# Kernel optimization log

Measured on AMD Instinct MI355X. Metric: run time of the kernel, lower is better.

## Reference

```python
import jax, jax.numpy as jnp
import numpy as np

N_NODES = 1_000_000
N_EDGES = 16_000_000
D = 2          # num_dimensions (hard-coded in source)
H = 64         # hidden_channnels
G = 1024       # number of graphs in the batch


def setup_inputs() -> dict:
    key = jax.random.key(0)
    ks = jax.random.split(key, 10)
    x = jax.random.normal(ks[0], (N_NODES, D), dtype=jnp.float32)
    edge_index = jax.random.randint(ks[1], (2, N_EDGES), 0, N_NODES, dtype=jnp.int64)
    batch = jnp.sort(jax.random.randint(ks[2], (N_NODES,), 0, G, dtype=jnp.int64))
    s = 0.5
    return {
        "x": x,
        "lin_w": jax.random.normal(ks[3], (D, D), dtype=jnp.float32) * s,
        "lin_b": jnp.zeros((D,), jnp.float32),
        "gn_weight": jnp.ones((D,), jnp.float32),
        "gn_bias": jnp.zeros((D,), jnp.float32),
        "gn_mean_scale": jnp.ones((D,), jnp.float32),
        "gcn_w": jax.random.normal(ks[4], (D, D), dtype=jnp.float32) * s,
        "gcn_b": jnp.zeros((D,), jnp.float32),
        "fc1_w": jax.random.normal(ks[5], (H, D), dtype=jnp.float32) * s,
        "fc1_b": jnp.zeros((H,), jnp.float32),
        "fc2_w": jax.random.normal(ks[6], (D, H), dtype=jnp.float32) * (1.0 / np.sqrt(H)),
        "fc2_b": jnp.zeros((D,), jnp.float32),
        "edge_index": edge_index,
        "batch": batch,
    }


def reference(x, lin_w, lin_b, gn_weight, gn_bias, gn_mean_scale,
              gcn_w, gcn_b, fc1_w, fc1_b, fc2_w, fc2_b, edge_index, batch):
    n = x.shape[0]
    # lin
    h = x @ lin_w.T + lin_b
    # GraphNorm called without batch -> single-graph stats; eps = num_dimensions = 2 (arg-order quirk)
    mean = h.mean(axis=0)
    out = h - mean * gn_mean_scale
    var = (out * out).mean(axis=0)
    h = gn_weight * out * jax.lax.rsqrt(var + jnp.float32(D)) + gn_bias
    h = jax.nn.relu(h)
    # GCNConv (add_self_loops=True, sym norm) + residual
    row, col = edge_index[0], edge_index[1]
    deg = jax.ops.segment_sum(jnp.ones_like(col, dtype=h.dtype), col, num_segments=n) + 1.0
    dis = jax.lax.rsqrt(deg)                       # deg^{-1/2}
    hw = h @ gcn_w.T                               # [N, D]
    msg = (dis[row] * dis[col])[:, None] * hw[row] # [E, D]
    agg = jax.ops.segment_sum(msg, col, num_segments=n)
    conv = agg + hw / deg[:, None] + gcn_b         # self-loop term = dis_i^2 * hw_i
    h = conv + h
    # fc1
    h = h @ fc1_w.T + fc1_b                        # [N, H]
    # InstanceNorm1d on 2D input -> unbatched (C=N, L=H): per-row norm over H; eps = H (arg-order quirk)
    m = h.mean(axis=1, keepdims=True)
    v = ((h - m) ** 2).mean(axis=1, keepdims=True)
    h = (h - m) * jax.lax.rsqrt(v + jnp.float32(H))
    # fc2
    h = h @ fc2_w.T + fc2_b                        # [N, D]
    # scatter_mean over batch
    ssum = jax.ops.segment_sum(h, batch, num_segments=G)
    cnt = jax.ops.segment_sum(jnp.ones((n,), h.dtype), batch, num_segments=G)
    return ssum / jnp.maximum(cnt, 1.0)[:, None]
```

## Files before the change

kernel.cpp:

```cpp
#include <hip/hip_runtime.h>

#define BLK 256
#define CH 8192
#define BSHIFT 12
#define BRANGE 4096
#define BMASK 4095
#define NSB 512


__global__ void k_stats_hist(const float* __restrict__ x, int n,
                             const int* __restrict__ col, int E, int NB,
                             double* __restrict__ partials, int* __restrict__ bhist) {
    __shared__ int h[256];
    for (int j = threadIdx.x; j < 256; j += blockDim.x) h[j] = 0;
    __syncthreads();
    int stride = gridDim.x * blockDim.x;
    int gtid = blockIdx.x * blockDim.x + threadIdx.x;

    int nqe = E >> 2;
    for (int q = gtid; q < nqe; q += stride) {
        int4 c = reinterpret_cast<const int4*>(col)[q];
        atomicAdd(&h[c.x >> BSHIFT], 1);
        atomicAdd(&h[c.y >> BSHIFT], 1);
        atomicAdd(&h[c.z >> BSHIFT], 1);
        atomicAdd(&h[c.w >> BSHIFT], 1);
    }
    if (blockIdx.x == 0) {
        for (int e = (nqe << 2) + threadIdx.x; e < E; e += blockDim.x)
            atomicAdd(&h[col[e] >> BSHIFT], 1);
    }

    float s0 = 0.f, s1 = 0.f, s2 = 0.f, s3 = 0.f, s4 = 0.f;
    int nv = n >> 1;
    for (int i = gtid; i < nv; i += stride) {
        float4 v = reinterpret_cast<const float4*>(x)[i];
        s0 += v.x + v.z; s1 += v.y + v.w;
        s2 += v.x * v.x + v.z * v.z;
        s3 += v.y * v.y + v.w * v.w;
        s4 += v.x * v.y + v.z * v.w;
    }
    if (blockIdx.x == 0 && threadIdx.x == 0 && (n & 1)) {
        float2 v = reinterpret_cast<const float2*>(x)[n - 1];
        s0 += v.x; s1 += v.y; s2 += v.x * v.x; s3 += v.y * v.y; s4 += v.x * v.y;
    }
    for (int off = 32; off; off >>= 1) {
        s0 += __shfl_down(s0, off);
        s1 += __shfl_down(s1, off);
        s2 += __shfl_down(s2, off);
        s3 += __shfl_down(s3, off);
        s4 += __shfl_down(s4, off);
    }
    __shared__ double lds[4][5];
    int wid = threadIdx.x >> 6;
    if ((threadIdx.x & 63) == 0) {
        lds[wid][0] = s0; lds[wid][1] = s1; lds[wid][2] = s2;
        lds[wid][3] = s3; lds[wid][4] = s4;
    }
    __syncthreads();
    if (threadIdx.x == 0) {
        double t0 = 0, t1 = 0, t2 = 0, t3 = 0, t4 = 0;
        for (int w = 0; w < 4; ++w) {
            t0 += lds[w][0]; t1 += lds[w][1]; t2 += lds[w][2];
            t3 += lds[w][3]; t4 += lds[w][4];
        }
        double* o = partials + (size_t)blockIdx.x * 5;
        o[0] = t0; o[1] = t1; o[2] = t2; o[3] = t3; o[4] = t4;
    }
    for (int j = threadIdx.x; j < NB; j += blockDim.x)
        if (h[j]) atomicAdd(&bhist[j], h[j]);
}


__global__ void k_params(const double* __restrict__ partials, int np,
                         const int* __restrict__ bhist, int NB,
                         int* __restrict__ gbase, int* __restrict__ cursor,
                         const float* lin_w, const float* lin_b,
                         const float* gn_w, const float* gn_b, const float* gn_ms,
                         const float* gcn_w, const float* gcn_b,
                         const float* fc1_w, const float* fc1_b,
                         const float* fc2_w, const float* fc2_b,
                         int n, float* __restrict__ P) {
    int tid = threadIdx.x;
    if (bhist) {
        __shared__ int si[256];
        int hv = (tid < NB) ? bhist[tid] : 0;
        si[tid] = hv; __syncthreads();
        for (int off = 1; off < 256; off <<= 1) {
            int t = (tid >= off) ? si[tid - off] : 0;
            __syncthreads();
            si[tid] += t;
            __syncthreads();
        }
        if (tid < NB) { gbase[tid] = si[tid] - hv; cursor[tid] = si[tid] - hv; }
        if (tid == 0) gbase[NB] = si[255];
        __syncthreads();
    }
    double a0 = 0, a1 = 0, a2 = 0, a3 = 0, a4 = 0;
    for (int i = tid; i < np; i += blockDim.x) {
        const double* q = partials + (size_t)i * 5;
        a0 += q[0]; a1 += q[1]; a2 += q[2]; a3 += q[3]; a4 += q[4];
    }
    for (int off = 32; off; off >>= 1) {
        a0 += __shfl_down(a0, off);
        a1 += __shfl_down(a1, off);
        a2 += __shfl_down(a2, off);
        a3 += __shfl_down(a3, off);
        a4 += __shfl_down(a4, off);
    }
    __shared__ double red[4][5];
    int wid = tid >> 6;
    if ((tid & 63) == 0) {
        red[wid][0] = a0; red[wid][1] = a1; red[wid][2] = a2;
        red[wid][3] = a3; red[wid][4] = a4;
    }
    __syncthreads();
    if (tid != 0) return;
    double Sx0 = 0, Sx1 = 0, Sxx = 0, Syy = 0, Sxy = 0;
    for (int w = 0; w < 4; ++w) {
        Sx0 += red[w][0]; Sx1 += red[w][1]; Sxx += red[w][2];
        Syy += red[w][3]; Sxy += red[w][4];
    }
    double N = (double)n;
    for (int c = 0; c < 2; ++c) {
        double L0 = lin_w[c * 2], L1 = lin_w[c * 2 + 1], lb = lin_b[c];
        double m   = (L0 * Sx0 + L1 * Sx1) / N + lb;
        double Eh2 = (L0 * L0 * Sxx + L1 * L1 * Syy + 2.0 * L0 * L1 * Sxy
                      + 2.0 * lb * (L0 * Sx0 + L1 * Sx1)) / N + lb * lb;
        double s   = gn_ms[c];
        double var = Eh2 - 2.0 * s * m * m + s * s * m * m;
        double inv = 1.0 / sqrt(var + 2.0);
        double gam = gn_w[c];
        P[c * 2 + 0] = (float)(gam * inv * L0);
        P[c * 2 + 1] = (float)(gam * inv * L1);
        P[4 + c]     = (float)(gam * inv * (lb - m * s) + gn_b[c]);
    }
    P[6] = gcn_w[0]; P[7] = gcn_w[1]; P[8] = gcn_w[2]; P[9] = gcn_w[3];
    P[10] = gcn_b[0]; P[11] = gcn_b[1];
    double b0 = 0, b1 = 0, bb = 0;
    for (int j = 0; j < 64; ++j) { b0 += fc1_w[2 * j]; b1 += fc1_w[2 * j + 1]; bb += fc1_b[j]; }
    b0 /= 64.0; b1 /= 64.0; bb /= 64.0;
    double S00 = 0, S01 = 0, S11 = 0, Sb0 = 0, Sb1 = 0, Sbb = 0;
    double M00 = 0, M01 = 0, M10 = 0, M11 = 0, t0 = 0, t1 = 0;
    for (int j = 0; j < 64; ++j) {
        double w0 = fc1_w[2 * j] - b0, w1 = fc1_w[2 * j + 1] - b1, b = fc1_b[j] - bb;
        S00 += w0 * w0; S01 += w0 * w1; S11 += w1 * w1;
        Sb0 += w0 * b;  Sb1 += w1 * b;  Sbb += b * b;
        double f0 = fc2_w[j], f1 = fc2_w[64 + j];
        M00 += f0 * w0; M01 += f0 * w1; t0 += f0 * b;
        M10 += f1 * w0; M11 += f1 * w1; t1 += f1 * b;
    }
    P[12] = (float)(S00 / 64.0); P[13] = (float)(S01 / 64.0); P[14] = (float)(S11 / 64.0);
    P[15] = (float)(Sb0 / 64.0); P[16] = (float)(Sb1 / 64.0); P[17] = (float)(Sbb / 64.0);
    P[18] = (float)M00; P[19] = (float)M01; P[20] = (float)M10; P[21] = (float)M11;
    P[22] = (float)t0;  P[23] = (float)t1;
    P[24] = fc2_b[0];   P[25] = fc2_b[1];
}


__global__ void k_hist(const int* __restrict__ col, int E, int NB, int* __restrict__ bhist) {
    __shared__ int h[256];
    for (int j = threadIdx.x; j < 256; j += blockDim.x) h[j] = 0;
    __syncthreads();
    int nq = E >> 2;
    int stride = gridDim.x * blockDim.x;
    for (int q = blockIdx.x * blockDim.x + threadIdx.x; q < nq; q += stride) {
        int4 c = reinterpret_cast<const int4*>(col)[q];
        atomicAdd(&h[c.x >> BSHIFT], 1);
        atomicAdd(&h[c.y >> BSHIFT], 1);
        atomicAdd(&h[c.z >> BSHIFT], 1);
        atomicAdd(&h[c.w >> BSHIFT], 1);
    }
    if (blockIdx.x == 0) {
        for (int e = (nq << 2) + threadIdx.x; e < E; e += blockDim.x)
            atomicAdd(&h[col[e] >> BSHIFT], 1);
    }
    __syncthreads();
    for (int j = threadIdx.x; j < NB; j += blockDim.x)
        if (h[j]) atomicAdd(&bhist[j], h[j]);
}

__global__ __launch_bounds__(256) void k_binA(const int* __restrict__ row,
                                              const int* __restrict__ col, int E,
                                              int NB, int* __restrict__ cursor,
                                              unsigned* __restrict__ staging) {
    __shared__ unsigned buf[CH];
    __shared__ int h[256], si[256], lpos[256], lcur[256];
    int tid = threadIdx.x;
    int start = blockIdx.x * CH;
    int end = start + CH; if (end > E) end = E;
    h[tid] = 0;
    __syncthreads();
    for (int e = start + tid; e < end; e += 256)
        atomicAdd(&h[col[e] >> BSHIFT], 1);
    __syncthreads();
    int hv = h[tid];
    si[tid] = hv; __syncthreads();
    for (int off = 1; off < 256; off <<= 1) {
        int t = (tid >= off) ? si[tid - off] : 0;
        __syncthreads();
        si[tid] += t;
        __syncthreads();
    }
    lpos[tid] = si[tid] - hv;
    lcur[tid] = (tid < NB && hv) ? atomicAdd(&cursor[tid], hv) : 0;
    __syncthreads();
    for (int e = start + tid; e < end; e += 256) {
        int c = col[e];
        unsigned w = ((unsigned)row[e] << BSHIFT) | (unsigned)(c & BMASK);
        int slot = atomicAdd(&lpos[c >> BSHIFT], 1);
        buf[slot] = w;
    }
    __syncthreads();
    int wid = tid >> 6, lane = tid & 63;
    for (int b = wid; b < NB; b += 4) {
        int m = h[b];
        if (!m) continue;
        int lb = si[b] - m;
        int g = lcur[b];
        for (int k = lane; k < m; k += 64)
            staging[g + k] = buf[lb + k];
    }
}

__global__ __launch_bounds__(1024) void k_degprep(const unsigned* __restrict__ staging,
                                                  const int* __restrict__ gbase,
                                                  const float* __restrict__ x,
                                                  const float* __restrict__ P,
                                                  int n, int* __restrict__ deg,
                                                  float2* __restrict__ p) {
    __shared__ int hist[BRANGE];
    int tid = threadIdx.x;
    for (int j = tid; j < BRANGE; j += 1024) hist[j] = 0;
    __syncthreads();
    int s = gbase[blockIdx.x], e = gbase[blockIdx.x + 1];
    int pre = (4 - (s & 3)) & 3; int cnt = e - s; if (pre > cnt) pre = cnt;
    for (int i = s + tid; i < s + pre; i += 1024)
        atomicAdd(&hist[staging[i] & BMASK], 1);
    int vs = s + pre;
    int nq = (e - vs) >> 2;
    const uint4* sv = reinterpret_cast<const uint4*>(staging + vs);
    for (int q = tid; q < nq; q += 1024) {
        uint4 w = sv[q];
        atomicAdd(&hist[w.x & BMASK], 1);
        atomicAdd(&hist[w.y & BMASK], 1);
        atomicAdd(&hist[w.z & BMASK], 1);
        atomicAdd(&hist[w.w & BMASK], 1);
    }
    for (int i = vs + (nq << 2) + tid; i < e; i += 1024)
        atomicAdd(&hist[staging[i] & BMASK], 1);
    __syncthreads();
    float A00 = P[0], A01 = P[1], A10 = P[2], A11 = P[3], q0 = P[4], q1 = P[5];
    float g00 = P[6], g01 = P[7], g10 = P[8], g11 = P[9];
    int nb = blockIdx.x << BSHIFT;
    int lim = n - nb; if (lim > BRANGE) lim = BRANGE;
    for (int j = tid; j < lim; j += 1024) {
        int d = hist[j];
        deg[nb + j] = d;
        float2 v = reinterpret_cast<const float2*>(x)[nb + j];
        float gg0 = fmaxf(fmaf(A00, v.x, fmaf(A01, v.y, q0)), 0.f);
        float gg1 = fmaxf(fmaf(A10, v.x, fmaf(A11, v.y, q1)), 0.f);
        float hw0 = g00 * gg0 + g01 * gg1;
        float hw1 = g10 * gg0 + g11 * gg1;
        float degf = (float)d + 1.0f;
        float dis = rsqrtf(degf);
        p[nb + j] = make_float2(dis * hw0, dis * hw1);
    }
}

#define AGG2(W, PV) \
    atomicAdd(&acc[2 * ((W) & BMASK)],     (PV).x); \
    atomicAdd(&acc[2 * ((W) & BMASK) + 1], (PV).y);

__global__ __launch_bounds__(1024) void k_agg(
        const unsigned* __restrict__ staging, const int* __restrict__ gbase,
        const float2* __restrict__ p, float* __restrict__ pacc) {
    __shared__ float acc[2 * BRANGE];
    int tid = threadIdx.x;
    for (int j = tid; j < 2 * BRANGE; j += 1024) acc[j] = 0.f;
    __syncthreads();
    int b = blockIdx.x >> 1, half = blockIdx.x & 1;
    int s0 = gbase[b], e0 = gbase[b + 1];
    int hc = (e0 - s0) >> 1;
    int s = s0 + half * hc;
    int e = half ? e0 : (s0 + hc);
    int cnt = e - s;
    int pre = (4 - (s & 3)) & 3; if (pre > cnt) pre = cnt;
    for (int i = s + tid; i < s + pre; i += 1024) {
        unsigned w = staging[i]; float2 pv = p[w >> BSHIFT];
        AGG2(w, pv)
    }
    int vs = s + pre;
    int nq = (e - vs) >> 2;
    const uint4* sv = reinterpret_cast<const uint4*>(staging + vs);
    int q = tid;
    for (; q + 3 * 1024 < nq; q += 4 * 1024) {
        uint4 wa = sv[q];
        uint4 wb = sv[q + 1024];
        uint4 wc = sv[q + 2048];
        uint4 wd = sv[q + 3072];
        float2 a0 = p[wa.x >> BSHIFT], a1 = p[wa.y >> BSHIFT];
        float2 a2 = p[wa.z >> BSHIFT], a3 = p[wa.w >> BSHIFT];
        float2 b0 = p[wb.x >> BSHIFT], b1 = p[wb.y >> BSHIFT];
        float2 b2 = p[wb.z >> BSHIFT], b3 = p[wb.w >> BSHIFT];
        float2 c0 = p[wc.x >> BSHIFT], c1 = p[wc.y >> BSHIFT];
        float2 c2 = p[wc.z >> BSHIFT], c3 = p[wc.w >> BSHIFT];
        float2 d0 = p[wd.x >> BSHIFT], d1 = p[wd.y >> BSHIFT];
        float2 d2 = p[wd.z >> BSHIFT], d3 = p[wd.w >> BSHIFT];
        AGG2(wa.x, a0) AGG2(wa.y, a1) AGG2(wa.z, a2) AGG2(wa.w, a3)
        AGG2(wb.x, b0) AGG2(wb.y, b1) AGG2(wb.z, b2) AGG2(wb.w, b3)
        AGG2(wc.x, c0) AGG2(wc.y, c1) AGG2(wc.z, c2) AGG2(wc.w, c3)
        AGG2(wd.x, d0) AGG2(wd.y, d1) AGG2(wd.z, d2) AGG2(wd.w, d3)
    }
    for (; q < nq; q += 1024) {
        uint4 w = sv[q];
        float2 p0 = p[w.x >> BSHIFT], p1 = p[w.y >> BSHIFT];
        float2 p2 = p[w.z >> BSHIFT], p3 = p[w.w >> BSHIFT];
        AGG2(w.x, p0) AGG2(w.y, p1) AGG2(w.z, p2) AGG2(w.w, p3)
    }
    for (int i = vs + (nq << 2) + tid; i < e; i += 1024) {
        unsigned w = staging[i]; float2 pv = p[w >> BSHIFT];
        AGG2(w, pv)
    }
    __syncthreads();
    float* pa = pacc + (size_t)blockIdx.x * (2 * BRANGE);
    for (int j = tid; j < 2 * BRANGE; j += 1024) pa[j] = acc[j];
}

__global__ __launch_bounds__(1024) void k_fin(
        const float* __restrict__ pacc, const float* __restrict__ x,
        const int* __restrict__ deg, const int* __restrict__ batch,
        const float* __restrict__ Pp, int n,
        float* __restrict__ gsum, float* __restrict__ gcnt) {
    int tid = threadIdx.x;
    int b = blockIdx.x;
    const float2* a0p = reinterpret_cast<const float2*>(pacc + (size_t)(2 * b)     * (2 * BRANGE));
    const float2* a1p = reinterpret_cast<const float2*>(pacc + (size_t)(2 * b + 1) * (2 * BRANGE));
    float A00 = Pp[0], A01 = Pp[1], A10 = Pp[2], A11 = Pp[3], q0f = Pp[4], q1f = Pp[5];
    float g00 = Pp[6], g01 = Pp[7], g10 = Pp[8], g11 = Pp[9];
    float gb0 = Pp[10], gb1 = Pp[11];
    float S00 = Pp[12], S01 = Pp[13], S11 = Pp[14], Sb0 = Pp[15], Sb1 = Pp[16], Sbb = Pp[17];
    float M00 = Pp[18], M01 = Pp[19], M10 = Pp[20], M11 = Pp[21];
    float t0 = Pp[22], t1 = Pp[23], fb0 = Pp[24], fb1 = Pp[25];
    int nb = b << BSHIFT;
    int lim = n - nb; if (lim > BRANGE) lim = BRANGE;
    for (int j = tid; j < lim; j += 1024) {
        int i = nb + j;
        float2 A = a0p[j], B = a1p[j];
        float a0v = A.x + B.x, a1v = A.y + B.y;
        float2 v = reinterpret_cast<const float2*>(x)[i];
        float g0 = fmaxf(fmaf(A00, v.x, fmaf(A01, v.y, q0f)), 0.f);
        float g1 = fmaxf(fmaf(A10, v.x, fmaf(A11, v.y, q1f)), 0.f);
        float hw0 = g00 * g0 + g01 * g1;
        float hw1 = g10 * g0 + g11 * g1;
        float degf = (float)deg[i] + 1.0f;
        float dis = rsqrtf(degf);
        float c0 = dis * a0v + hw0 / degf + gb0 + g0;
        float c1 = dis * a1v + hw1 / degf + gb1 + g1;
        float vq = S00 * c0 * c0 + 2.f * S01 * c0 * c1 + S11 * c1 * c1
                 + 2.f * Sb0 * c0 + 2.f * Sb1 * c1 + Sbb;
        float inv = rsqrtf(vq + 64.0f);
        float o0 = inv * (M00 * c0 + M01 * c1 + t0) + fb0;
        float o1 = inv * (M10 * c0 + M11 * c1 + t1) + fb1;
        int bg = batch[i];
        int b0 = __shfl(bg, 0);
        if (__all(bg == b0)) {
            float s0 = o0, s1 = o1;
            for (int off = 32; off; off >>= 1) {
                s0 += __shfl_down(s0, off);
                s1 += __shfl_down(s1, off);
            }
            if ((tid & 63) == 0) {
                atomicAdd(&gsum[2 * b0], s0);
                atomicAdd(&gsum[2 * b0 + 1], s1);
                atomicAdd(&gcnt[b0], 64.0f);
            }
        } else {
            atomicAdd(&gsum[2 * bg], o0);
            atomicAdd(&gsum[2 * bg + 1], o1);
            atomicAdd(&gcnt[bg], 1.0f);
        }
    }
}

__global__ void k_div(const float* __restrict__ gsum, const float* __restrict__ gcnt,
                      float* __restrict__ out, int G) {
    int g = blockIdx.x * blockDim.x + threadIdx.x;
    if (g < G) {
        float c = fmaxf(gcnt[g], 1.0f);
        out[2 * g]     = gsum[2 * g] / c;
        out[2 * g + 1] = gsum[2 * g + 1] / c;
    }
}


__global__ void k_stats(const float* __restrict__ x, int n, double* __restrict__ partials) {
    float s0 = 0.f, s1 = 0.f, s2 = 0.f, s3 = 0.f, s4 = 0.f;
    int nv = n >> 1;
    int stride = gridDim.x * blockDim.x;
    for (int i = blockIdx.x * blockDim.x + threadIdx.x; i < nv; i += stride) {
        float4 v = reinterpret_cast<const float4*>(x)[i];
        s0 += v.x + v.z; s1 += v.y + v.w;
        s2 += v.x * v.x + v.z * v.z;
        s3 += v.y * v.y + v.w * v.w;
        s4 += v.x * v.y + v.z * v.w;
    }
    if (blockIdx.x == 0 && threadIdx.x == 0 && (n & 1)) {
        float2 v = reinterpret_cast<const float2*>(x)[n - 1];
        s0 += v.x; s1 += v.y; s2 += v.x * v.x; s3 += v.y * v.y; s4 += v.x * v.y;
    }
    for (int off = 32; off; off >>= 1) {
        s0 += __shfl_down(s0, off);
        s1 += __shfl_down(s1, off);
        s2 += __shfl_down(s2, off);
        s3 += __shfl_down(s3, off);
        s4 += __shfl_down(s4, off);
    }
    __shared__ double lds[4][5];
    int wid = threadIdx.x >> 6;
    if ((threadIdx.x & 63) == 0) {
        lds[wid][0] = s0; lds[wid][1] = s1; lds[wid][2] = s2;
        lds[wid][3] = s3; lds[wid][4] = s4;
    }
    __syncthreads();
    if (threadIdx.x == 0) {
        double t0 = 0, t1 = 0, t2 = 0, t3 = 0, t4 = 0;
        for (int w = 0; w < 4; ++w) {
            t0 += lds[w][0]; t1 += lds[w][1]; t2 += lds[w][2];
            t3 += lds[w][3]; t4 += lds[w][4];
        }
        double* o = partials + (size_t)blockIdx.x * 5;
        o[0] = t0; o[1] = t1; o[2] = t2; o[3] = t3; o[4] = t4;
    }
}

__global__ void k_prep(const float* __restrict__ x, const int* __restrict__ deg,
                       const float* __restrict__ P, int n, float2* __restrict__ p) {
    int stride = gridDim.x * blockDim.x;
    float A00 = P[0], A01 = P[1], A10 = P[2], A11 = P[3], q0 = P[4], q1 = P[5];
    float g00 = P[6], g01 = P[7], g10 = P[8], g11 = P[9];
    for (int i = blockIdx.x * blockDim.x + threadIdx.x; i < n; i += stride) {
        float2 v = reinterpret_cast<const float2*>(x)[i];
        float g0 = fmaxf(fmaf(A00, v.x, fmaf(A01, v.y, q0)), 0.f);
        float g1 = fmaxf(fmaf(A10, v.x, fmaf(A11, v.y, q1)), 0.f);
        float hw0 = g00 * g0 + g01 * g1;
        float hw1 = g10 * g0 + g11 * g1;
        float degf = (float)deg[i] + 1.0f;
        float dis = rsqrtf(degf);
        p[i] = make_float2(dis * hw0, dis * hw1);
    }
}

__global__ void k_deg(const int* __restrict__ col, int E, int* __restrict__ deg) {
    int nq = (E + 3) >> 2;
    int q = blockIdx.x * blockDim.x + threadIdx.x;
    if (q >= nq) return;
    int base = q << 2;
    if (base + 3 < E) {
        int4 c = reinterpret_cast<const int4*>(col)[q];
        atomicAdd(&deg[c.x], 1); atomicAdd(&deg[c.y], 1);
        atomicAdd(&deg[c.z], 1); atomicAdd(&deg[c.w], 1);
    } else {
        for (int e = base; e < E; ++e) atomicAdd(&deg[col[e]], 1);
    }
}

__global__ void k_edge(const int* __restrict__ row, const int* __restrict__ col, int E,
                       const float2* __restrict__ p, float* __restrict__ agg) {
    int nq = (E + 3) >> 2;
    int q = blockIdx.x * blockDim.x + threadIdx.x;
    if (q >= nq) return;
    int base = q << 2;
    if (base + 3 < E) {
        int4 r = reinterpret_cast<const int4*>(row)[q];
        int4 c = reinterpret_cast<const int4*>(col)[q];
        float2 p0 = p[r.x], p1 = p[r.y], p2 = p[r.z], p3 = p[r.w];
        atomicAdd(&agg[2 * c.x], p0.x); atomicAdd(&agg[2 * c.x + 1], p0.y);
        atomicAdd(&agg[2 * c.y], p1.x); atomicAdd(&agg[2 * c.y + 1], p1.y);
        atomicAdd(&agg[2 * c.z], p2.x); atomicAdd(&agg[2 * c.z + 1], p2.y);
        atomicAdd(&agg[2 * c.w], p3.x); atomicAdd(&agg[2 * c.w + 1], p3.y);
    } else {
        for (int e = base; e < E; ++e) {
            float2 pv = p[row[e]];
            atomicAdd(&agg[2 * col[e]], pv.x);
            atomicAdd(&agg[2 * col[e] + 1], pv.y);
        }
    }
}

__global__ void k_final(const float* __restrict__ x, const int* __restrict__ deg,
                        const float* __restrict__ agg, const int* __restrict__ batch,
                        const float* __restrict__ P, int n,
                        float* __restrict__ gsum, float* __restrict__ gcnt) {
    int i = blockIdx.x * blockDim.x + threadIdx.x;
    bool valid = i < n;
    float A00 = P[0], A01 = P[1], A10 = P[2], A11 = P[3], q0 = P[4], q1 = P[5];
    float g00 = P[6], g01 = P[7], g10 = P[8], g11 = P[9];
    float gb0 = P[10], gb1 = P[11];
    float S00 = P[12], S01 = P[13], S11 = P[14], Sb0 = P[15], Sb1 = P[16], Sbb = P[17];
    float M00 = P[18], M01 = P[19], M10 = P[20], M11 = P[21];
    float t0 = P[22], t1 = P[23], fb0 = P[24], fb1 = P[25];

    float o0 = 0.f, o1 = 0.f;
    int b = 0;
    if (valid) {
        float2 v = reinterpret_cast<const float2*>(x)[i];
        float g0 = fmaxf(fmaf(A00, v.x, fmaf(A01, v.y, q0)), 0.f);
        float g1 = fmaxf(fmaf(A10, v.x, fmaf(A11, v.y, q1)), 0.f);
        float hw0 = g00 * g0 + g01 * g1;
        float hw1 = g10 * g0 + g11 * g1;
        float degf = (float)deg[i] + 1.0f;
        float dis = rsqrtf(degf);
        float a0 = agg[2 * i], a1 = agg[2 * i + 1];
        float c0 = dis * a0 + hw0 / degf + gb0 + g0;
        float c1 = dis * a1 + hw1 / degf + gb1 + g1;
        float vq = S00 * c0 * c0 + 2.f * S01 * c0 * c1 + S11 * c1 * c1
                 + 2.f * Sb0 * c0 + 2.f * Sb1 * c1 + Sbb;
        float inv = rsqrtf(vq + 64.0f);
        o0 = inv * (M00 * c0 + M01 * c1 + t0) + fb0;
        o1 = inv * (M10 * c0 + M11 * c1 + t1) + fb1;
        b = batch[i];
    }
    unsigned long long act = __ballot(valid);
    if (act == ~0ull) {
        int b0 = __shfl(b, 0);
        if (__all(b == b0)) {
            float s0 = o0, s1 = o1;
            for (int off = 32; off; off >>= 1) {
                s0 += __shfl_down(s0, off);
                s1 += __shfl_down(s1, off);
            }
            if ((threadIdx.x & 63) == 0) {
                atomicAdd(&gsum[2 * b0], s0);
                atomicAdd(&gsum[2 * b0 + 1], s1);
                atomicAdd(&gcnt[b0], 64.0f);
            }
        } else {
            atomicAdd(&gsum[2 * b], o0);
            atomicAdd(&gsum[2 * b + 1], o1);
            atomicAdd(&gcnt[b], 1.0f);
        }
    } else if (valid) {
        atomicAdd(&gsum[2 * b], o0);
        atomicAdd(&gsum[2 * b + 1], o1);
        atomicAdd(&gcnt[b], 1.0f);
    }
}


extern "C" void kernel_launch(void* const* d_in, const int* in_sizes, int n_in,
                              void* d_out, int out_size, void* d_ws, size_t ws_size,
                              hipStream_t stream) {
    const float* x      = (const float*)d_in[0];
    const float* lin_w  = (const float*)d_in[1];
    const float* lin_b  = (const float*)d_in[2];
    const float* gn_w   = (const float*)d_in[3];
    const float* gn_b   = (const float*)d_in[4];
    const float* gn_ms  = (const float*)d_in[5];
    const float* gcn_w  = (const float*)d_in[6];
    const float* gcn_b  = (const float*)d_in[7];
    const float* fc1_w  = (const float*)d_in[8];
    const float* fc1_b  = (const float*)d_in[9];
    const float* fc2_w  = (const float*)d_in[10];
    const float* fc2_b  = (const float*)d_in[11];
    const int*   ei     = (const int*)d_in[12];
    const int*   batch  = (const int*)d_in[13];

    int n = in_sizes[0] / 2;
    int E = in_sizes[12] / 2;
    int G = out_size / 2;
    const int* row = ei;
    const int* col = ei + E;

    char* ws = (char*)d_ws;
    int nb_nodes = (n + BLK - 1) / BLK;
    int NB = (n + BRANGE - 1) >> BSHIFT;

    size_t zero_end  = 16384 + (size_t)12 * G;
    size_t part_off  = (zero_end + 255) & ~(size_t)255;
    size_t deg_off   = (part_off + (size_t)40 * NSB + 255) & ~(size_t)255;
    size_t p_off     = deg_off + (size_t)4 * n;
    size_t pacc_off  = p_off + (size_t)8 * n;
    size_t stag_off  = pacc_off + (size_t)NB * 2 * (2 * BRANGE) * 4;
    size_t need      = stag_off + (size_t)4 * E;

    bool fast = (n <= (1 << 20)) && (NB <= 253) && (need <= ws_size) &&
                (zero_end <= 16384 + 12288);

    if (fast) {
        float*    P       = (float*)(ws + 64);
        int*      bhist   = (int*)(ws + 4096);
        int*      gbase   = (int*)(ws + 8192);
        int*      cursor  = (int*)(ws + 12288);
        float*    gsum    = (float*)(ws + 16384);
        float*    gcnt    = (float*)(ws + 16384 + (size_t)8 * G);
        double*   part    = (double*)(ws + part_off);
        int*      deg     = (int*)(ws + deg_off);
        float2*   p       = (float2*)(ws + p_off);
        float*    pacc    = (float*)(ws + pacc_off);
        unsigned* staging = (unsigned*)(ws + stag_off);

        hipMemsetAsync(d_ws, 0, zero_end, stream);

        int nbinA = (E + CH - 1) / CH;

        k_stats_hist<<<NSB, BLK, 0, stream>>>(x, n, col, E, NB, part, bhist);
        k_params<<<1, 256, 0, stream>>>(part, NSB, bhist, NB, gbase, cursor,
                                        lin_w, lin_b, gn_w, gn_b, gn_ms,
                                        gcn_w, gcn_b, fc1_w, fc1_b, fc2_w, fc2_b, n, P);
        k_binA<<<nbinA, 256, 0, stream>>>(row, col, E, NB, cursor, staging);
        k_degprep<<<NB, 1024, 0, stream>>>(staging, gbase, x, P, n, deg, p);
        k_agg<<<NB * 2, 1024, 0, stream>>>(staging, gbase, p, pacc);
        k_fin<<<NB, 1024, 0, stream>>>(pacc, x, deg, batch, P, n, gsum, gcnt);
        k_div<<<(G + BLK - 1) / BLK, BLK, 0, stream>>>(gsum, gcnt, (float*)d_out, G);
    } else {
        float*  P     = (float*)(ws + 64);
        float*  gsum  = (float*)(ws + 4096);
        float*  gcnt  = (float*)(ws + 4096 + (size_t)8 * G);
        size_t fzero_end = 4096 + (size_t)12 * G;
        size_t fpart_off = (fzero_end + 255) & ~(size_t)255;
        size_t fdeg_off  = (fpart_off + (size_t)40 * NSB + 255) & ~(size_t)255;
        int*    deg   = (int*)(ws + fdeg_off);
        size_t fagg_off = fdeg_off + (size_t)4 * n;
        float*  agg   = (float*)(ws + fagg_off);
        size_t fp_off = fagg_off + (size_t)8 * n;
        float2* p     = (float2*)(ws + fp_off);
        double* part  = (double*)(ws + fpart_off);

        hipMemsetAsync(ws + 4096, 0, fzero_end - 4096, stream);
        hipMemsetAsync(ws + fdeg_off, 0, (size_t)12 * n, stream);

        int nq = (E + 3) >> 2;
        int nb_edge = (nq + BLK - 1) / BLK;

        k_stats<<<NSB, BLK, 0, stream>>>(x, n, part);
        k_deg<<<nb_edge, BLK, 0, stream>>>(col, E, deg);
        k_params<<<1, 256, 0, stream>>>(part, NSB, (const int*)nullptr, 0,
                                        (int*)nullptr, (int*)nullptr,
                                        lin_w, lin_b, gn_w, gn_b, gn_ms,
                                        gcn_w, gcn_b, fc1_w, fc1_b, fc2_w, fc2_b, n, P);
        k_prep<<<nb_nodes, BLK, 0, stream>>>(x, deg, P, n, p);
        k_edge<<<nb_edge, BLK, 0, stream>>>(row, col, E, p, agg);
        k_final<<<nb_nodes, BLK, 0, stream>>>(x, deg, agg, batch, P, n, gsum, gcnt);
        k_div<<<(G + BLK - 1) / BLK, BLK, 0, stream>>>(gsum, gcnt, (float*)d_out, G);
    }
}
```

Measured before the change: 377.8 us.

## Sort edges by source segment in degprep and fuse aggregation with finalize

k_degprep now also partitions each destination bucket's edges into four source-node segments, writing them to a second staging buffer with per-block offsets. Grouping edges by source range is meant to give the gathers of p better cache locality. k_agg and k_fin are merged into k_aggfin, which keeps the accumulator in shared memory and drops the pacc round trip through global memory. The cost is an extra read and write pass over staging, ballot-based scatter work, and half as many blocks during aggregation.

After: 477.9 us. 1.27x slower.

```diff
diff --git a/kernel.cpp b/kernel.cpp
--- a/kernel.cpp
+++ b/kernel.cpp
@@ -5,6 +5,7 @@
 #define BSHIFT 12
 #define BRANGE 4096
 #define BMASK 4095
+#define NSEG 4
 #define NSB 512
 
 
@@ -157,28 +158,6 @@
 }
 
 
-__global__ void k_hist(const int* __restrict__ col, int E, int NB, int* __restrict__ bhist) {
-    __shared__ int h[256];
-    for (int j = threadIdx.x; j < 256; j += blockDim.x) h[j] = 0;
-    __syncthreads();
-    int nq = E >> 2;
-    int stride = gridDim.x * blockDim.x;
-    for (int q = blockIdx.x * blockDim.x + threadIdx.x; q < nq; q += stride) {
-        int4 c = reinterpret_cast<const int4*>(col)[q];
-        atomicAdd(&h[c.x >> BSHIFT], 1);
-        atomicAdd(&h[c.y >> BSHIFT], 1);
-        atomicAdd(&h[c.z >> BSHIFT], 1);
-        atomicAdd(&h[c.w >> BSHIFT], 1);
-    }
-    if (blockIdx.x == 0) {
-        for (int e = (nq << 2) + threadIdx.x; e < E; e += blockDim.x)
-            atomicAdd(&h[col[e] >> BSHIFT], 1);
-    }
-    __syncthreads();
-    for (int j = threadIdx.x; j < NB; j += blockDim.x)
-        if (h[j]) atomicAdd(&bhist[j], h[j]);
-}
-
 __global__ __launch_bounds__(256) void k_binA(const int* __restrict__ row,
                                               const int* __restrict__ col, int E,
                                               int NB, int* __restrict__ cursor,
@@ -226,29 +205,66 @@
                                                   const int* __restrict__ gbase,
                                                   const float* __restrict__ x,
                                                   const float* __restrict__ P,
-                                                  int n, int* __restrict__ deg,
+                                                  int n, int segshift, int do_sort,
+                                                  unsigned* __restrict__ staging2,
+                                                  int* __restrict__ soff,
+                                                  int* __restrict__ deg,
                                                   float2* __restrict__ p) {
     __shared__ int hist[BRANGE];
+    __shared__ int segc[NSEG], segcur[NSEG];
     int tid = threadIdx.x;
+    int lane = tid & 63;
+    unsigned long long ltmask = (1ull << lane) - 1;
     for (int j = tid; j < BRANGE; j += 1024) hist[j] = 0;
+    if (tid < NSEG) segc[tid] = 0;
     __syncthreads();
     int s = gbase[blockIdx.x], e = gbase[blockIdx.x + 1];
-    int pre = (4 - (s & 3)) & 3; int cnt = e - s; if (pre > cnt) pre = cnt;
-    for (int i = s + tid; i < s + pre; i += 1024)
-        atomicAdd(&hist[staging[i] & BMASK], 1);
-    int vs = s + pre;
-    int nq = (e - vs) >> 2;
-    const uint4* sv = reinterpret_cast<const uint4*>(staging + vs);
-    for (int q = tid; q < nq; q += 1024) {
-        uint4 w = sv[q];
-        atomicAdd(&hist[w.x & BMASK], 1);
-        atomicAdd(&hist[w.y & BMASK], 1);
-        atomicAdd(&hist[w.z & BMASK], 1);
-        atomicAdd(&hist[w.w & BMASK], 1);
-    }
-    for (int i = vs + (nq << 2) + tid; i < e; i += 1024)
-        atomicAdd(&hist[staging[i] & BMASK], 1);
-    __syncthreads();
+
+    for (int i = s + tid; i < e; i += 1024) {
+        unsigned w = staging[i];
+        atomicAdd(&hist[w & BMASK], 1);
+        if (do_sort) {
+            int sg = (int)((w >> BSHIFT) >> segshift);
+            #pragma unroll
+            for (int s2 = 0; s2 < NSEG; ++s2) {
+                unsigned long long m = __ballot(sg == s2);
+                if (sg == s2 && __popcll(m & ltmask) == 0)
+                    atomicAdd(&segc[s2], (int)__popcll(m));
+            }
+        }
+    }
+    __syncthreads();
+
+    if (do_sort) {
+        if (tid == 0) {
+            int a = 0;
+            for (int s2 = 0; s2 < NSEG; ++s2) {
+                soff[blockIdx.x * (NSEG + 1) + s2] = a;
+                segcur[s2] = a;
+                a += segc[s2];
+            }
+            soff[blockIdx.x * (NSEG + 1) + NSEG] = a;
+        }
+        __syncthreads();
+        for (int i = s + tid; i < e; i += 1024) {
+            unsigned w = staging[i];
+            int sg = (int)((w >> BSHIFT) >> segshift);
+            #pragma unroll
+            for (int s2 = 0; s2 < NSEG; ++s2) {
+                unsigned long long m = __ballot(sg == s2);
+                if (sg == s2) {
+                    int prel = (int)__popcll(m & ltmask);
+                    int ldr = (int)__ffsll((unsigned long long)m) - 1;
+                    int base_ = 0;
+                    if (prel == 0) base_ = atomicAdd(&segcur[s2], (int)__popcll(m));
+                    base_ = __shfl(base_, ldr);
+                    staging2[s + base_ + prel] = w;
+                }
+            }
+        }
+    }
+    __syncthreads();
+
     float A00 = P[0], A01 = P[1], A10 = P[2], A11 = P[3], q0 = P[4], q1 = P[5];
     float g00 = P[6], g01 = P[7], g10 = P[8], g11 = P[9];
     int nb = blockIdx.x << BSHIFT;
@@ -271,33 +287,25 @@
     atomicAdd(&acc[2 * ((W) & BMASK)],     (PV).x); \
     atomicAdd(&acc[2 * ((W) & BMASK) + 1], (PV).y);
 
-__global__ __launch_bounds__(1024) void k_agg(
-        const unsigned* __restrict__ staging, const int* __restrict__ gbase,
-        const float2* __restrict__ p, float* __restrict__ pacc) {
-    __shared__ float acc[2 * BRANGE];
-    int tid = threadIdx.x;
-    for (int j = tid; j < 2 * BRANGE; j += 1024) acc[j] = 0.f;
-    __syncthreads();
-    int b = blockIdx.x >> 1, half = blockIdx.x & 1;
-    int s0 = gbase[b], e0 = gbase[b + 1];
-    int hc = (e0 - s0) >> 1;
-    int s = s0 + half * hc;
-    int e = half ? e0 : (s0 + hc);
-    int cnt = e - s;
-    int pre = (4 - (s & 3)) & 3; if (pre > cnt) pre = cnt;
-    for (int i = s + tid; i < s + pre; i += 1024) {
+__device__ __forceinline__ void agg_range(const unsigned* __restrict__ staging,
+                                          int rs, int re,
+                                          const float2* __restrict__ p,
+                                          float* acc, int tid) {
+    int cnt = re - rs;
+    int pre = (4 - (rs & 3)) & 3; if (pre > cnt) pre = cnt;
+    for (int i = rs + tid; i < rs + pre; i += 1024) {
         unsigned w = staging[i]; float2 pv = p[w >> BSHIFT];
         AGG2(w, pv)
     }
-    int vs = s + pre;
-    int nq = (e - vs) >> 2;
+    int vs = rs + pre;
+    int nq = (re - vs) >> 2;
     const uint4* sv = reinterpret_cast<const uint4*>(staging + vs);
-    int q = tid;
-    for (; q + 3 * 1024 < nq; q += 4 * 1024) {
+    int qtr = nq >> 2;
+    for (int q = tid; q < qtr; q += 1024) {
         uint4 wa = sv[q];
-        uint4 wb = sv[q + 1024];
-        uint4 wc = sv[q + 2048];
-        uint4 wd = sv[q + 3072];
+        uint4 wb = sv[q + qtr];
+        uint4 wc = sv[q + 2 * qtr];
+        uint4 wd = sv[q + 3 * qtr];
         float2 a0 = p[wa.x >> BSHIFT], a1 = p[wa.y >> BSHIFT];
         float2 a2 = p[wa.z >> BSHIFT], a3 = p[wa.w >> BSHIFT];
         float2 b0 = p[wb.x >> BSHIFT], b1 = p[wb.y >> BSHIFT];
@@ -311,42 +319,48 @@
         AGG2(wc.x, c0) AGG2(wc.y, c1) AGG2(wc.z, c2) AGG2(wc.w, c3)
         AGG2(wd.x, d0) AGG2(wd.y, d1) AGG2(wd.z, d2) AGG2(wd.w, d3)
     }
-    for (; q < nq; q += 1024) {
+    for (int q = (qtr << 2) + tid; q < nq; q += 1024) {
         uint4 w = sv[q];
         float2 p0 = p[w.x >> BSHIFT], p1 = p[w.y >> BSHIFT];
         float2 p2 = p[w.z >> BSHIFT], p3 = p[w.w >> BSHIFT];
         AGG2(w.x, p0) AGG2(w.y, p1) AGG2(w.z, p2) AGG2(w.w, p3)
     }
-    for (int i = vs + (nq << 2) + tid; i < e; i += 1024) {
+    for (int i = vs + (nq << 2) + tid; i < re; i += 1024) {
         unsigned w = staging[i]; float2 pv = p[w >> BSHIFT];
         AGG2(w, pv)
     }
-    __syncthreads();
-    float* pa = pacc + (size_t)blockIdx.x * (2 * BRANGE);
-    for (int j = tid; j < 2 * BRANGE; j += 1024) pa[j] = acc[j];
-}
-
-__global__ __launch_bounds__(1024) void k_fin(
-        const float* __restrict__ pacc, const float* __restrict__ x,
-        const int* __restrict__ deg, const int* __restrict__ batch,
-        const float* __restrict__ Pp, int n,
+}
+
+__global__ __launch_bounds__(1024) void k_aggfin(
+        const unsigned* __restrict__ staging, const int* __restrict__ gbase,
+        const int* __restrict__ soff, const float2* __restrict__ p,
+        const float* __restrict__ x, const int* __restrict__ deg,
+        const int* __restrict__ batch, const float* __restrict__ Pp, int n,
         float* __restrict__ gsum, float* __restrict__ gcnt) {
+    __shared__ float acc[2 * BRANGE];
     int tid = threadIdx.x;
-    int b = blockIdx.x;
-    const float2* a0p = reinterpret_cast<const float2*>(pacc + (size_t)(2 * b)     * (2 * BRANGE));
-    const float2* a1p = reinterpret_cast<const float2*>(pacc + (size_t)(2 * b + 1) * (2 * BRANGE));
+    for (int j = tid; j < 2 * BRANGE; j += 1024) acc[j] = 0.f;
+    __syncthreads();
+    int gb = gbase[blockIdx.x];
+    if (soff) {
+        const int* so = soff + blockIdx.x * (NSEG + 1);
+        for (int s = 0; s < NSEG; ++s)
+            agg_range(staging, gb + so[s], gb + so[s + 1], p, acc, tid);
+    } else {
+        agg_range(staging, gb, gbase[blockIdx.x + 1], p, acc, tid);
+    }
+    __syncthreads();
+
     float A00 = Pp[0], A01 = Pp[1], A10 = Pp[2], A11 = Pp[3], q0f = Pp[4], q1f = Pp[5];
     float g00 = Pp[6], g01 = Pp[7], g10 = Pp[8], g11 = Pp[9];
     float gb0 = Pp[10], gb1 = Pp[11];
     float S00 = Pp[12], S01 = Pp[13], S11 = Pp[14], Sb0 = Pp[15], Sb1 = Pp[16], Sbb = Pp[17];
     float M00 = Pp[18], M01 = Pp[19], M10 = Pp[20], M11 = Pp[21];
     float t0 = Pp[22], t1 = Pp[23], fb0 = Pp[24], fb1 = Pp[25];
-    int nb = b << BSHIFT;
+    int nb = blockIdx.x << BSHIFT;
     int lim = n - nb; if (lim > BRANGE) lim = BRANGE;
     for (int j = tid; j < lim; j += 1024) {
         int i = nb + j;
-        float2 A = a0p[j], B = a1p[j];
-        float a0v = A.x + B.x, a1v = A.y + B.y;
         float2 v = reinterpret_cast<const float2*>(x)[i];
         float g0 = fmaxf(fmaf(A00, v.x, fmaf(A01, v.y, q0f)), 0.f);
         float g1 = fmaxf(fmaf(A10, v.x, fmaf(A11, v.y, q1f)), 0.f);
@@ -354,6 +368,7 @@
         float hw1 = g10 * g0 + g11 * g1;
         float degf = (float)deg[i] + 1.0f;
         float dis = rsqrtf(degf);
+        float a0v = acc[2 * j], a1v = acc[2 * j + 1];
         float c0 = dis * a0v + hw0 / degf + gb0 + g0;
         float c1 = dis * a1v + hw1 / degf + gb1 + g1;
         float vq = S00 * c0 * c0 + 2.f * S01 * c0 * c1 + S11 * c1 * c1
@@ -574,30 +589,37 @@
     char* ws = (char*)d_ws;
     int nb_nodes = (n + BLK - 1) / BLK;
     int NB = (n + BRANGE - 1) >> BSHIFT;
+    int segshift = 0;
+    while (((unsigned)(n - 1) >> segshift) >= (unsigned)NSEG) ++segshift;
 
     size_t zero_end  = 16384 + (size_t)12 * G;
     size_t part_off  = (zero_end + 255) & ~(size_t)255;
-    size_t deg_off   = (part_off + (size_t)40 * NSB + 255) & ~(size_t)255;
+    size_t soff_off  = (part_off + (size_t)40 * NSB + 255) & ~(size_t)255;
+    size_t deg_off   = (soff_off + (size_t)4 * (NSEG + 1) * (NB + 1) + 255) & ~(size_t)255;
     size_t p_off     = deg_off + (size_t)4 * n;
-    size_t pacc_off  = p_off + (size_t)8 * n;
-    size_t stag_off  = pacc_off + (size_t)NB * 2 * (2 * BRANGE) * 4;
-    size_t need      = stag_off + (size_t)4 * E;
+    size_t stag_off  = p_off + (size_t)8 * n;
+    size_t stag2_off = stag_off + (size_t)4 * E;
+    size_t need      = stag2_off + (size_t)4 * E;
+
+    int do_sort = 1;
+    if (need > ws_size) { do_sort = 0; need = stag_off + (size_t)4 * E; }
 
     bool fast = (n <= (1 << 20)) && (NB <= 253) && (need <= ws_size) &&
                 (zero_end <= 16384 + 12288);
 
     if (fast) {
-        float*    P       = (float*)(ws + 64);
-        int*      bhist   = (int*)(ws + 4096);
-        int*      gbase   = (int*)(ws + 8192);
-        int*      cursor  = (int*)(ws + 12288);
-        float*    gsum    = (float*)(ws + 16384);
-        float*    gcnt    = (float*)(ws + 16384 + (size_t)8 * G);
-        double*   part    = (double*)(ws + part_off);
-        int*      deg     = (int*)(ws + deg_off);
-        float2*   p       = (float2*)(ws + p_off);
-        float*    pacc    = (float*)(ws + pacc_off);
-        unsigned* staging = (unsigned*)(ws + stag_off);
+        float*    P        = (float*)(ws + 64);
+        int*      bhist    = (int*)(ws + 4096);
+        int*      gbase    = (int*)(ws + 8192);
+        int*      cursor   = (int*)(ws + 12288);
+        float*    gsum     = (float*)(ws + 16384);
+        float*    gcnt     = (float*)(ws + 16384 + (size_t)8 * G);
+        double*   part     = (double*)(ws + part_off);
+        int*      soff     = (int*)(ws + soff_off);
+        int*      deg      = (int*)(ws + deg_off);
+        float2*   p        = (float2*)(ws + p_off);
+        unsigned* staging  = (unsigned*)(ws + stag_off);
+        unsigned* staging2 = do_sort ? (unsigned*)(ws + stag2_off) : (unsigned*)(ws + stag_off);
 
         hipMemsetAsync(d_ws, 0, zero_end, stream);
 
@@ -608,9 +630,10 @@
                                         lin_w, lin_b, gn_w, gn_b, gn_ms,
                                         gcn_w, gcn_b, fc1_w, fc1_b, fc2_w, fc2_b, n, P);
         k_binA<<<nbinA, 256, 0, stream>>>(row, col, E, NB, cursor, staging);
-        k_degprep<<<NB, 1024, 0, stream>>>(staging, gbase, x, P, n, deg, p);
-        k_agg<<<NB * 2, 1024, 0, stream>>>(staging, gbase, p, pacc);
-        k_fin<<<NB, 1024, 0, stream>>>(pacc, x, deg, batch, P, n, gsum, gcnt);
+        k_degprep<<<NB, 1024, 0, stream>>>(staging, gbase, x, P, n, segshift, do_sort,
+                                           staging2, soff, deg, p);
+        k_aggfin<<<NB, 1024, 0, stream>>>(staging2, gbase, do_sort ? soff : (int*)nullptr,
+                                          p, x, deg, batch, P, n, gsum, gcnt);
         k_div<<<(G + BLK - 1) / BLK, BLK, 0, stream>>>(gsum, gcnt, (float*)d_out, G);
     } else {
         float*  P     = (float*)(ws + 64);
```

## Fuse aggregation and finalize kernels, keeping per-bucket accumulators in LDS

Applied to the files above, without the earlier changes.

Merges the edge aggregation kernel and the node finalize kernel into one, so accumulated messages are read directly from shared memory instead of being written to and reread from a global partial buffer. This removes the partial-accumulator global traffic and one kernel launch. In exchange each bucket is handled by a single block rather than two halves, halving the grid and doubling per-block edge work, which may reduce parallelism across CUs. A ballot check is added so the wave-level reduction only runs when all lanes are active.

Result: faster. 368.5 us (-2.4%).

```diff
diff --git a/kernel.cpp b/kernel.cpp
--- a/kernel.cpp
+++ b/kernel.cpp
@@ -271,18 +271,17 @@
     atomicAdd(&acc[2 * ((W) & BMASK)],     (PV).x); \
     atomicAdd(&acc[2 * ((W) & BMASK) + 1], (PV).y);
 
-__global__ __launch_bounds__(1024) void k_agg(
+__global__ __launch_bounds__(1024) void k_aggfin(
         const unsigned* __restrict__ staging, const int* __restrict__ gbase,
-        const float2* __restrict__ p, float* __restrict__ pacc) {
+        const float2* __restrict__ p, const float* __restrict__ x,
+        const int* __restrict__ deg, const int* __restrict__ batch,
+        const float* __restrict__ Pp, int n,
+        float* __restrict__ gsum, float* __restrict__ gcnt) {
     __shared__ float acc[2 * BRANGE];
     int tid = threadIdx.x;
     for (int j = tid; j < 2 * BRANGE; j += 1024) acc[j] = 0.f;
     __syncthreads();
-    int b = blockIdx.x >> 1, half = blockIdx.x & 1;
-    int s0 = gbase[b], e0 = gbase[b + 1];
-    int hc = (e0 - s0) >> 1;
-    int s = s0 + half * hc;
-    int e = half ? e0 : (s0 + hc);
+    int s = gbase[blockIdx.x], e = gbase[blockIdx.x + 1];
     int cnt = e - s;
     int pre = (4 - (s & 3)) & 3; if (pre > cnt) pre = cnt;
     for (int i = s + tid; i < s + pre; i += 1024) {
@@ -322,31 +321,17 @@
         AGG2(w, pv)
     }
     __syncthreads();
-    float* pa = pacc + (size_t)blockIdx.x * (2 * BRANGE);
-    for (int j = tid; j < 2 * BRANGE; j += 1024) pa[j] = acc[j];
-}
-
-__global__ __launch_bounds__(1024) void k_fin(
-        const float* __restrict__ pacc, const float* __restrict__ x,
-        const int* __restrict__ deg, const int* __restrict__ batch,
-        const float* __restrict__ Pp, int n,
-        float* __restrict__ gsum, float* __restrict__ gcnt) {
-    int tid = threadIdx.x;
-    int b = blockIdx.x;
-    const float2* a0p = reinterpret_cast<const float2*>(pacc + (size_t)(2 * b)     * (2 * BRANGE));
-    const float2* a1p = reinterpret_cast<const float2*>(pacc + (size_t)(2 * b + 1) * (2 * BRANGE));
+
     float A00 = Pp[0], A01 = Pp[1], A10 = Pp[2], A11 = Pp[3], q0f = Pp[4], q1f = Pp[5];
     float g00 = Pp[6], g01 = Pp[7], g10 = Pp[8], g11 = Pp[9];
     float gb0 = Pp[10], gb1 = Pp[11];
     float S00 = Pp[12], S01 = Pp[13], S11 = Pp[14], Sb0 = Pp[15], Sb1 = Pp[16], Sbb = Pp[17];
     float M00 = Pp[18], M01 = Pp[19], M10 = Pp[20], M11 = Pp[21];
     float t0 = Pp[22], t1 = Pp[23], fb0 = Pp[24], fb1 = Pp[25];
-    int nb = b << BSHIFT;
+    int nb = blockIdx.x << BSHIFT;
     int lim = n - nb; if (lim > BRANGE) lim = BRANGE;
     for (int j = tid; j < lim; j += 1024) {
         int i = nb + j;
-        float2 A = a0p[j], B = a1p[j];
-        float a0v = A.x + B.x, a1v = A.y + B.y;
         float2 v = reinterpret_cast<const float2*>(x)[i];
         float g0 = fmaxf(fmaf(A00, v.x, fmaf(A01, v.y, q0f)), 0.f);
         float g1 = fmaxf(fmaf(A10, v.x, fmaf(A11, v.y, q1f)), 0.f);
@@ -354,6 +339,7 @@
         float hw1 = g10 * g0 + g11 * g1;
         float degf = (float)deg[i] + 1.0f;
         float dis = rsqrtf(degf);
+        float a0v = acc[2 * j], a1v = acc[2 * j + 1];
         float c0 = dis * a0v + hw0 / degf + gb0 + g0;
         float c1 = dis * a1v + hw1 / degf + gb1 + g1;
         float vq = S00 * c0 * c0 + 2.f * S01 * c0 * c1 + S11 * c1 * c1
@@ -362,17 +348,24 @@
         float o0 = inv * (M00 * c0 + M01 * c1 + t0) + fb0;
         float o1 = inv * (M10 * c0 + M11 * c1 + t1) + fb1;
         int bg = batch[i];
-        int b0 = __shfl(bg, 0);
-        if (__all(bg == b0)) {
-            float s0 = o0, s1 = o1;
-            for (int off = 32; off; off >>= 1) {
-                s0 += __shfl_down(s0, off);
-                s1 += __shfl_down(s1, off);
-            }
-            if ((tid & 63) == 0) {
-                atomicAdd(&gsum[2 * b0], s0);
-                atomicAdd(&gsum[2 * b0 + 1], s1);
-                atomicAdd(&gcnt[b0], 64.0f);
+        unsigned long long act = __ballot(true);
+        if (act == ~0ull) {
+            int b0 = __shfl(bg, 0);
+            if (__all(bg == b0)) {
+                float s0 = o0, s1 = o1;
+                for (int off = 32; off; off >>= 1) {
+                    s0 += __shfl_down(s0, off);
+                    s1 += __shfl_down(s1, off);
+                }
+                if ((tid & 63) == 0) {
+                    atomicAdd(&gsum[2 * b0], s0);
+                    atomicAdd(&gsum[2 * b0 + 1], s1);
+                    atomicAdd(&gcnt[b0], 64.0f);
+                }
+            } else {
+                atomicAdd(&gsum[2 * bg], o0);
+                atomicAdd(&gsum[2 * bg + 1], o1);
+                atomicAdd(&gcnt[bg], 1.0f);
             }
         } else {
             atomicAdd(&gsum[2 * bg], o0);
@@ -579,8 +572,7 @@
     size_t part_off  = (zero_end + 255) & ~(size_t)255;
     size_t deg_off   = (part_off + (size_t)40 * NSB + 255) & ~(size_t)255;
     size_t p_off     = deg_off + (size_t)4 * n;
-    size_t pacc_off  = p_off + (size_t)8 * n;
-    size_t stag_off  = pacc_off + (size_t)NB * 2 * (2 * BRANGE) * 4;
+    size_t stag_off  = p_off + (size_t)8 * n;
     size_t need      = stag_off + (size_t)4 * E;
 
     bool fast = (n <= (1 << 20)) && (NB <= 253) && (need <= ws_size) &&
@@ -596,7 +588,6 @@
         double*   part    = (double*)(ws + part_off);
         int*      deg     = (int*)(ws + deg_off);
         float2*   p       = (float2*)(ws + p_off);
-        float*    pacc    = (float*)(ws + pacc_off);
         unsigned* staging = (unsigned*)(ws + stag_off);
 
         hipMemsetAsync(d_ws, 0, zero_end, stream);
@@ -609,8 +600,8 @@
                                         gcn_w, gcn_b, fc1_w, fc1_b, fc2_w, fc2_b, n, P);
         k_binA<<<nbinA, 256, 0, stream>>>(row, col, E, NB, cursor, staging);
         k_degprep<<<NB, 1024, 0, stream>>>(staging, gbase, x, P, n, deg, p);
-        k_agg<<<NB * 2, 1024, 0, stream>>>(staging, gbase, p, pacc);
-        k_fin<<<NB, 1024, 0, stream>>>(pacc, x, deg, batch, P, n, gsum, gcnt);
+        k_aggfin<<<NB, 1024, 0, stream>>>(staging, gbase, p, x, deg, batch,
+                                          P, n, gsum, gcnt);
         k_div<<<(G + BLK - 1) / BLK, BLK, 0, stream>>>(gsum, gcnt, (float*)d_out, G);
     } else {
         float*  P     = (float*)(ws + 64);
```
